# Kernel optimization log

Hardware: AMD Instinct MI355X
Metric: run time of the kernel (lower is better)

Reference implementation:

```python
import jax, jax.numpy as jnp
import numpy as np

N_STUDENT = 100000
N_COURSE = 20000
N_EDGES = 1000000
HIDDEN = 128


def setup_inputs() -> dict:
    key = jax.random.key(0)
    ks = jax.random.split(key, 8)
    scale = 1.0 / np.sqrt(2 * HIDDEN)
    return {
        "z_student": jax.random.normal(ks[0], (N_STUDENT, HIDDEN), dtype=jnp.float32),
        "z_course": jax.random.normal(ks[1], (N_COURSE, HIDDEN), dtype=jnp.float32),
        "row": jax.random.randint(ks[2], (N_EDGES,), 0, N_STUDENT, dtype=jnp.int64),
        "col": jax.random.randint(ks[3], (N_EDGES,), 0, N_COURSE, dtype=jnp.int64),
        "W1": jax.random.normal(ks[4], (2 * HIDDEN, HIDDEN), dtype=jnp.float32) * scale,
        "b1": jnp.zeros((HIDDEN,), dtype=jnp.float32),
        "W2": jax.random.normal(ks[5], (HIDDEN, 1), dtype=jnp.float32) * (1.0 / np.sqrt(HIDDEN)),
        "b2": jnp.zeros((1,), dtype=jnp.float32),
    }


def reference(z_student, z_course, row, col, W1, b1, W2, b2):
    # gather endpoint embeddings and concat along feature dim: [E, 2H]
    z = jnp.concatenate([z_student[row], z_course[col]], axis=-1)
    h = jax.nn.relu(z @ W1 + b1)   # [E, H]
    out = h @ W2 + b2              # [E, 1]
    return out.reshape(-1)
```

## Files before the change

### kernel.cpp

```cpp
#include <hip/hip_runtime.h>
#include <hip/hip_bf16.h>


typedef __attribute__((ext_vector_type(8))) short short8;
typedef __attribute__((ext_vector_type(4))) float float4v;

static __device__ __forceinline__ unsigned short f32_to_bf16(float f) {
    union { float f; unsigned u; } v; v.f = f;
    unsigned r = v.u + 0x7fffu + ((v.u >> 16) & 1u);
    return (unsigned short)(r >> 16);
}
static __device__ __forceinline__ float bf16_lo(unsigned u) {
    union { unsigned u; float f; } v; v.u = u << 16; return v.f;
}
static __device__ __forceinline__ float bf16_hi(unsigned u) {
    union { unsigned u; float f; } v; v.u = u & 0xffff0000u; return v.f;
}

__global__ void conv_w_kernel(const float* __restrict__ W1, unsigned short* __restrict__ Wt) {
    int id = blockIdx.x * 256 + threadIdx.x;
    int h = id >> 14;
    int n = (id >> 7) & 127;
    int k = id & 127;
    Wt[id] = f32_to_bf16(W1[(h * 128 + k) * 128 + n]);
}

#define LDSPITCH 136
__global__ __launch_bounds__(256) void gemm_u_kernel(
    const float* __restrict__ Z, const unsigned short* __restrict__ Wt,
    const float* __restrict__ b1, unsigned short* __restrict__ U,
    int M, int addB)
{
    __shared__ __align__(16) unsigned short lds[128 * LDSPITCH];
    const int tid = threadIdx.x;

    for (int i = 0; i < 8; ++i) {
        int j = tid + i * 256;
        int n = j >> 4, chunk = j & 15;
        uint4 v = ((const uint4*)Wt)[j];
        *((uint4*)&lds[n * LDSPITCH + chunk * 8]) = v;
    }
    __syncthreads();

    const int wave = tid >> 6, lane = tid & 63;
    const int quad = lane >> 4, l16 = lane & 15;
    long mrow = (long)blockIdx.x * 64 + wave * 16 + l16;
    long mload = mrow < M ? mrow : (long)(M - 1);
    const float* zrow = Z + mload * 128;

    float4v acc[8];
    for (int nt = 0; nt < 8; ++nt) acc[nt] = (float4v)(0.0f);

    for (int c = 0; c < 4; ++c) {
        const float4* pa = (const float4*)(zrow + c * 32 + quad * 8);
        float4 a0 = pa[0], a1 = pa[1];
        short8 afrag;
        afrag[0] = (short)f32_to_bf16(a0.x); afrag[1] = (short)f32_to_bf16(a0.y);
        afrag[2] = (short)f32_to_bf16(a0.z); afrag[3] = (short)f32_to_bf16(a0.w);
        afrag[4] = (short)f32_to_bf16(a1.x); afrag[5] = (short)f32_to_bf16(a1.y);
        afrag[6] = (short)f32_to_bf16(a1.z); afrag[7] = (short)f32_to_bf16(a1.w);
        for (int nt = 0; nt < 8; ++nt) {
            const short8* pb = (const short8*)&lds[(nt * 16 + l16) * LDSPITCH + c * 32 + quad * 8];
            acc[nt] = __builtin_amdgcn_mfma_f32_16x16x32_bf16(afrag, *pb, acc[nt], 0, 0, 0);
        }
    }

    long rbase = (long)blockIdx.x * 64 + wave * 16 + quad * 4;
    for (int nt = 0; nt < 8; ++nt) {
        int n = nt * 16 + l16;
        float bv = addB ? b1[n] : 0.0f;
        for (int r = 0; r < 4; ++r) {
            long rr = rbase + r;
            if (rr < M) U[rr * 128 + n] = f32_to_bf16(acc[nt][r] + bv);
        }
    }
}

__global__ __launch_bounds__(256) void edge_kernel(
    const int* __restrict__ row, const int* __restrict__ col,
    const unsigned short* __restrict__ us, const unsigned short* __restrict__ uc,
    const float* __restrict__ w2, const float* __restrict__ b2,
    float* __restrict__ out, int E)
{
    const int tid = threadIdx.x;
    const int sub = tid & 15;
    long e = (long)blockIdx.x * 16 + (tid >> 4);
    if (e >= E) return;
    int r = row[e], c = col[e];

    uint4 av = *(const uint4*)(us + (long)r * 128 + sub * 8);
    uint4 bv = *(const uint4*)(uc + (long)c * 128 + sub * 8);
    const float4* pw = (const float4*)(w2 + sub * 8);
    float4 w0 = pw[0], w1 = pw[1];

    float a[8] = { bf16_lo(av.x), bf16_hi(av.x), bf16_lo(av.y), bf16_hi(av.y),
                   bf16_lo(av.z), bf16_hi(av.z), bf16_lo(av.w), bf16_hi(av.w) };
    float b[8] = { bf16_lo(bv.x), bf16_hi(bv.x), bf16_lo(bv.y), bf16_hi(bv.y),
                   bf16_lo(bv.z), bf16_hi(bv.z), bf16_lo(bv.w), bf16_hi(bv.w) };
    float w[8] = { w0.x, w0.y, w0.z, w0.w, w1.x, w1.y, w1.z, w1.w };

    float s = 0.0f;
    #pragma unroll
    for (int j = 0; j < 8; ++j) {
        float h = a[j] + b[j];
        h = h > 0.0f ? h : 0.0f;
        s += h * w[j];
    }
    s += __shfl_xor(s, 1);
    s += __shfl_xor(s, 2);
    s += __shfl_xor(s, 4);
    s += __shfl_xor(s, 8);
    if (sub == 0) out[e] = s + b2[0];
}

extern "C" void kernel_launch(void* const* d_in, const int* in_sizes, int n_in,
                              void* d_out, int out_size, void* d_ws, size_t ws_size,
                              hipStream_t stream) {
    const float* zs  = (const float*)d_in[0];
    const float* zc  = (const float*)d_in[1];
    const int*   row = (const int*)d_in[2];
    const int*   col = (const int*)d_in[3];
    const float* W1  = (const float*)d_in[4];
    const float* b1  = (const float*)d_in[5];
    const float* W2  = (const float*)d_in[6];
    const float* b2  = (const float*)d_in[7];
    float* out = (float*)d_out;

    const int Ms = in_sizes[0] / 128;
    const int Mc = in_sizes[1] / 128;
    const int E  = in_sizes[2];

    unsigned short* Wt = (unsigned short*)d_ws;
    unsigned short* us = (unsigned short*)((char*)d_ws + 65536);
    unsigned short* uc = us + (size_t)Ms * 128;

    conv_w_kernel<<<128, 256, 0, stream>>>(W1, Wt);
    gemm_u_kernel<<<(Ms + 63) / 64, 256, 0, stream>>>(zs, Wt,         b1, us, Ms, 1);
    gemm_u_kernel<<<(Mc + 63) / 64, 256, 0, stream>>>(zc, Wt + 16384, b1, uc, Mc, 0);
    edge_kernel<<<(E + 15) / 16, 256, 0, stream>>>(row, col, us, uc, W2, b2, out, E);
}
```

Before: 189.8 us.

## Switch to fp16 intermediates, merge GEMM launches, swizzle LDS, widen edge loads

Replaces the bf16 path with fp16: inputs are converted with the packed round-toward-zero instruction and the fp16 MFMA is used. The two per-table GEMM launches become one launch, the weight transpose goes through LDS, and the weight tile in LDS uses an XOR swizzle with output columns reordered so each lane stores 8 contiguous halves. The edge kernel handles 32 edges per block with 8 lanes each, uses packed half add/max and one fewer shuffle. fp16 has a narrower range than bf16 and the conversion truncates, which may change accuracy.

Result: faster. 169.6 us (-10.7%).

```diff
diff --git a/kernel.cpp b/kernel.cpp
--- a/kernel.cpp
+++ b/kernel.cpp
@@ -1,115 +1,148 @@
 #include <hip/hip_runtime.h>
 #include <hip/hip_bf16.h>
+#include <hip/hip_fp16.h>
 
 
-typedef __attribute__((ext_vector_type(8))) short short8;
-typedef __attribute__((ext_vector_type(4))) float float4v;
+typedef _Float16 half2v __attribute__((ext_vector_type(2)));
+typedef _Float16 half8v __attribute__((ext_vector_type(8)));
+typedef __fp16   fp16x2 __attribute__((ext_vector_type(2)));
+typedef float    float4v __attribute__((ext_vector_type(4)));
 
-static __device__ __forceinline__ unsigned short f32_to_bf16(float f) {
-    union { float f; unsigned u; } v; v.f = f;
-    unsigned r = v.u + 0x7fffu + ((v.u >> 16) & 1u);
-    return (unsigned short)(r >> 16);
-}
-static __device__ __forceinline__ float bf16_lo(unsigned u) {
-    union { unsigned u; float f; } v; v.u = u << 16; return v.f;
-}
-static __device__ __forceinline__ float bf16_hi(unsigned u) {
-    union { unsigned u; float f; } v; v.u = u & 0xffff0000u; return v.f;
+__global__ __launch_bounds__(256) void conv_w(const float* __restrict__ W1,
+                                              const float* __restrict__ W2,
+                                              _Float16* __restrict__ Wt,
+                                              _Float16* __restrict__ w2h) {
+    int b = blockIdx.x, t = threadIdx.x;
+    if (b == 8) { if (t < 128) w2h[t] = (_Float16)W2[t]; return; }
+    __shared__ _Float16 lds[32][136];
+    int h = b >> 2, n0 = (b & 3) * 32;
+    for (int i = 0; i < 16; ++i) {
+        int idx = i * 256 + t;
+        int k = idx >> 5, nn = idx & 31;
+        lds[nn][k] = (_Float16)W1[(h * 128 + k) * 128 + n0 + nn];
+    }
+    __syncthreads();
+    for (int j = 0; j < 2; ++j) {
+        int idx = j * 256 + t;
+        int nn = idx >> 4, kc = idx & 15;
+        half8v v;
+        #pragma unroll
+        for (int q = 0; q < 8; ++q) v[q] = lds[nn][kc * 8 + q];
+        *(half8v*)&Wt[((h * 128 + n0 + nn) * 128) + kc * 8] = v;
+    }
 }
 
-__global__ void conv_w_kernel(const float* __restrict__ W1, unsigned short* __restrict__ Wt) {
-    int id = blockIdx.x * 256 + threadIdx.x;
-    int h = id >> 14;
-    int n = (id >> 7) & 127;
-    int k = id & 127;
-    Wt[id] = f32_to_bf16(W1[(h * 128 + k) * 128 + n]);
-}
+__global__ __launch_bounds__(256) void gemm_u(
+    const float* __restrict__ Zs, const float* __restrict__ Zc,
+    const _Float16* __restrict__ Wt, const float* __restrict__ b1,
+    _Float16* __restrict__ Us, _Float16* __restrict__ Uc,
+    int Ms, int Mc, int nbs)
+{
+    __shared__ uint4 ldsW[2048];
+    const int bid = blockIdx.x, t = threadIdx.x;
 
-#define LDSPITCH 136
-__global__ __launch_bounds__(256) void gemm_u_kernel(
-    const float* __restrict__ Z, const unsigned short* __restrict__ Wt,
-    const float* __restrict__ b1, unsigned short* __restrict__ U,
-    int M, int addB)
-{
-    __shared__ __align__(16) unsigned short lds[128 * LDSPITCH];
-    const int tid = threadIdx.x;
+    const float* Z; _Float16* U; const _Float16* W; int M, m0, addB;
+    if (bid < nbs) { Z = Zs; U = Us; M = Ms; m0 = bid * 64;         W = Wt;         addB = 1; }
+    else           { Z = Zc; U = Uc; M = Mc; m0 = (bid - nbs) * 64; W = Wt + 16384; addB = 0; }
 
+    const uint4* Wv = (const uint4*)W;
+    #pragma unroll
     for (int i = 0; i < 8; ++i) {
-        int j = tid + i * 256;
-        int n = j >> 4, chunk = j & 15;
-        uint4 v = ((const uint4*)Wt)[j];
-        *((uint4*)&lds[n * LDSPITCH + chunk * 8]) = v;
+        int j = i * 256 + t;
+        int n = j >> 4, ch = j & 15;
+        ldsW[n * 16 + (ch ^ ((n >> 3) & 7))] = Wv[j];
     }
     __syncthreads();
 
-    const int wave = tid >> 6, lane = tid & 63;
-    const int quad = lane >> 4, l16 = lane & 15;
-    long mrow = (long)blockIdx.x * 64 + wave * 16 + l16;
-    long mload = mrow < M ? mrow : (long)(M - 1);
-    const float* zrow = Z + mload * 128;
+    const int wave = t >> 6, lane = t & 63, quad = lane >> 4, l16 = lane & 15;
+    int mrow = m0 + wave * 16 + l16;
+    int mload = mrow < M ? mrow : M - 1;
+    const float* zrow = Z + (long)mload * 128;
 
     float4v acc[8];
+    #pragma unroll
     for (int nt = 0; nt < 8; ++nt) acc[nt] = (float4v)(0.0f);
 
+    #pragma unroll
     for (int c = 0; c < 4; ++c) {
-        const float4* pa = (const float4*)(zrow + c * 32 + quad * 8);
-        float4 a0 = pa[0], a1 = pa[1];
-        short8 afrag;
-        afrag[0] = (short)f32_to_bf16(a0.x); afrag[1] = (short)f32_to_bf16(a0.y);
-        afrag[2] = (short)f32_to_bf16(a0.z); afrag[3] = (short)f32_to_bf16(a0.w);
-        afrag[4] = (short)f32_to_bf16(a1.x); afrag[5] = (short)f32_to_bf16(a1.y);
-        afrag[6] = (short)f32_to_bf16(a1.z); afrag[7] = (short)f32_to_bf16(a1.w);
+        const float4v* pa = (const float4v*)(zrow + c * 32 + quad * 8);
+        float4v a0 = pa[0], a1 = pa[1];
+        fp16x2 p[4];
+        p[0] = __builtin_amdgcn_cvt_pkrtz(a0[0], a0[1]);
+        p[1] = __builtin_amdgcn_cvt_pkrtz(a0[2], a0[3]);
+        p[2] = __builtin_amdgcn_cvt_pkrtz(a1[0], a1[1]);
+        p[3] = __builtin_amdgcn_cvt_pkrtz(a1[2], a1[3]);
+        half8v af;
+        __builtin_memcpy(&af, &p[0], 16);
+        const int ch = c * 4 + quad;
+        #pragma unroll
         for (int nt = 0; nt < 8; ++nt) {
-            const short8* pb = (const short8*)&lds[(nt * 16 + l16) * LDSPITCH + c * 32 + quad * 8];
-            acc[nt] = __builtin_amdgcn_mfma_f32_16x16x32_bf16(afrag, *pb, acc[nt], 0, 0, 0);
+            const int n = l16 * 8 + nt;
+            const half8v* pb = (const half8v*)&ldsW[n * 16 + (ch ^ (l16 & 7))];
+            acc[nt] = __builtin_amdgcn_mfma_f32_16x16x32_f16(af, *pb, acc[nt], 0, 0, 0);
         }
     }
 
-    long rbase = (long)blockIdx.x * 64 + wave * 16 + quad * 4;
-    for (int nt = 0; nt < 8; ++nt) {
-        int n = nt * 16 + l16;
-        float bv = addB ? b1[n] : 0.0f;
-        for (int r = 0; r < 4; ++r) {
-            long rr = rbase + r;
-            if (rr < M) U[rr * 128 + n] = f32_to_bf16(acc[nt][r] + bv);
+    float bv[8];
+    if (addB) {
+        const float4v* pb1 = (const float4v*)(b1 + l16 * 8);
+        float4v x0 = pb1[0], x1 = pb1[1];
+        bv[0]=x0[0]; bv[1]=x0[1]; bv[2]=x0[2]; bv[3]=x0[3];
+        bv[4]=x1[0]; bv[5]=x1[1]; bv[6]=x1[2]; bv[7]=x1[3];
+    } else {
+        #pragma unroll
+        for (int i = 0; i < 8; ++i) bv[i] = 0.0f;
+    }
+
+    const int rbase = m0 + wave * 16 + quad * 4;
+    #pragma unroll
+    for (int r = 0; r < 4; ++r) {
+        int rr = rbase + r;
+        if (rr < M) {
+            half8v o;
+            #pragma unroll
+            for (int nt = 0; nt < 8; ++nt) o[nt] = (_Float16)(acc[nt][r] + bv[nt]);
+            *(half8v*)&U[(long)rr * 128 + l16 * 8] = o;
         }
     }
 }
 
 __global__ __launch_bounds__(256) void edge_kernel(
     const int* __restrict__ row, const int* __restrict__ col,
-    const unsigned short* __restrict__ us, const unsigned short* __restrict__ uc,
-    const float* __restrict__ w2, const float* __restrict__ b2,
+    const _Float16* __restrict__ us, const _Float16* __restrict__ uc,
+    const _Float16* __restrict__ w2h, const float* __restrict__ b2,
     float* __restrict__ out, int E)
 {
-    const int tid = threadIdx.x;
-    const int sub = tid & 15;
-    long e = (long)blockIdx.x * 16 + (tid >> 4);
+    const int t = threadIdx.x;
+    const int sub = t & 7;
+    long e = (long)blockIdx.x * 32 + (t >> 3);
     if (e >= E) return;
     int r = row[e], c = col[e];
 
-    uint4 av = *(const uint4*)(us + (long)r * 128 + sub * 8);
-    uint4 bv = *(const uint4*)(uc + (long)c * 128 + sub * 8);
-    const float4* pw = (const float4*)(w2 + sub * 8);
-    float4 w0 = pw[0], w1 = pw[1];
+    const uint4* pa = (const uint4*)(us  + (long)r * 128 + sub * 16);
+    const uint4* pb = (const uint4*)(uc  + (long)c * 128 + sub * 16);
+    const uint4* pw = (const uint4*)(w2h + sub * 16);
+    uint4 a0 = pa[0], a1 = pa[1];
+    uint4 c0 = pb[0], c1 = pb[1];
+    uint4 w0 = pw[0], w1 = pw[1];
 
-    float a[8] = { bf16_lo(av.x), bf16_hi(av.x), bf16_lo(av.y), bf16_hi(av.y),
-                   bf16_lo(av.z), bf16_hi(av.z), bf16_lo(av.w), bf16_hi(av.w) };
-    float b[8] = { bf16_lo(bv.x), bf16_hi(bv.x), bf16_lo(bv.y), bf16_hi(bv.y),
-                   bf16_lo(bv.z), bf16_hi(bv.z), bf16_lo(bv.w), bf16_hi(bv.w) };
-    float w[8] = { w0.x, w0.y, w0.z, w0.w, w1.x, w1.y, w1.z, w1.w };
+    half2v A[8], B[8], W[8];
+    *(uint4*)&A[0] = a0; *(uint4*)&A[4] = a1;
+    *(uint4*)&B[0] = c0; *(uint4*)&B[4] = c1;
+    *(uint4*)&W[0] = w0; *(uint4*)&W[4] = w1;
 
+    const half2v zero = {(_Float16)0, (_Float16)0};
     float s = 0.0f;
     #pragma unroll
-    for (int j = 0; j < 8; ++j) {
-        float h = a[j] + b[j];
-        h = h > 0.0f ? h : 0.0f;
-        s += h * w[j];
+    for (int i = 0; i < 8; ++i) {
+        half2v h = A[i] + B[i];
+        h = __builtin_elementwise_max(h, zero);
+        s += (float)h[0] * (float)W[i][0];
+        s += (float)h[1] * (float)W[i][1];
     }
     s += __shfl_xor(s, 1);
     s += __shfl_xor(s, 2);
     s += __shfl_xor(s, 4);
-    s += __shfl_xor(s, 8);
     if (sub == 0) out[e] = s + b2[0];
 }
 
@@ -130,12 +163,14 @@
     const int Mc = in_sizes[1] / 128;
     const int E  = in_sizes[2];
 
-    unsigned short* Wt = (unsigned short*)d_ws;
-    unsigned short* us = (unsigned short*)((char*)d_ws + 65536);
-    unsigned short* uc = us + (size_t)Ms * 128;
+    _Float16* Wt  = (_Float16*)d_ws;
+    _Float16* w2h = (_Float16*)((char*)d_ws + 65536);
+    _Float16* us  = (_Float16*)((char*)d_ws + 65536 + 256);
+    _Float16* uc  = us + (size_t)Ms * 128;
 
-    conv_w_kernel<<<128, 256, 0, stream>>>(W1, Wt);
-    gemm_u_kernel<<<(Ms + 63) / 64, 256, 0, stream>>>(zs, Wt,         b1, us, Ms, 1);
-    gemm_u_kernel<<<(Mc + 63) / 64, 256, 0, stream>>>(zc, Wt + 16384, b1, uc, Mc, 0);
-    edge_kernel<<<(E + 15) / 16, 256, 0, stream>>>(row, col, us, uc, W2, b2, out, E);
+    const int nbs = (Ms + 63) / 64, nbc = (Mc + 63) / 64;
+
+    conv_w<<<9, 256, 0, stream>>>(W1, W2, Wt, w2h);
+    gemm_u<<<nbs + nbc, 256, 0, stream>>>(zs, zc, Wt, b1, us, uc, Ms, Mc, nbs);
+    edge_kernel<<<(E + 31) / 32, 256, 0, stream>>>(row, col, us, uc, w2h, b2, out, E);
 }
```
